# Kernel tuning notes

Hardware: AMD Instinct MI355X
Metric: run time of the kernel (lower is better)

## Reference

```python
import jax, jax.numpy as jnp
import numpy as np
from jax.scipy.special import logsumexp

B, T = 8192, 1024  # batch, timesteps; n_states = 2 (BKT: not-know / know)


def setup_inputs() -> dict:
    key = jax.random.key(0)
    k1, k2, k3 = jax.random.split(key, 3)
    corr = jax.random.randint(k1, (B, T), 0, 2)  # binary observations
    dynamics_logits = jax.random.normal(k2, (B, 3), dtype=jnp.float32)  # (pL, pF, pI0) logits
    obs_logits = jax.random.normal(k3, (B, T, 2), dtype=jnp.float32)  # (pG, pS) logits per step
    return {"corr": corr, "dynamics_logits": dynamics_logits, "obs_logits": obs_logits}


def _get_logits(dynamics_logits, obs_logits):
    # trans_logits[b] = [[0, d1],[d0, 0]]  (target, source)
    z = jnp.zeros_like(dynamics_logits[:, 0])
    trans_logits = jnp.stack([z, dynamics_logits[:, 1], dynamics_logits[:, 0], z], axis=1).reshape(-1, 2, 2)
    # obs_full[b,t] = [[0, o0],[o1, 0]]  (state, output)
    zo = jnp.zeros_like(obs_logits[:, :, 0])
    obs_full = jnp.stack([zo, obs_logits[:, :, 0], obs_logits[:, :, 1], zo], axis=2)
    obs_full = obs_full.reshape(obs_logits.shape[0], -1, 2, 2)
    # init_logits[b] = [0, d2]
    init_logits = jnp.stack([z, dynamics_logits[:, 2]], axis=1)
    return trans_logits, obs_full, init_logits


def _bkt(corr, dynamics_logits, obs_logits):
    trans_logits, obs_full, init_logits = _get_logits(dynamics_logits, obs_logits)
    log_obs = jax.nn.log_softmax(obs_full, axis=3)   # (B,T,2,2)
    log_t = jax.nn.log_softmax(trans_logits, axis=1)  # (B,2,2) softmax over target state
    log_alpha0 = jax.nn.log_softmax(init_logits, axis=1)  # (B,2)
    lo_t = jnp.moveaxis(log_obs, 1, 0)  # (T,B,2,2)
    y_t = corr.T                        # (T,B)

    def fwd_step(log_alpha, inp):
        lo, y = inp  # lo: (B,2,2), y: (B,)
        # predictive p(y_t | y_1:t-1)
        log_py_pred = logsumexp(lo + log_alpha[:, :, None], axis=1)  # (B,2)
        log_py_pred = log_py_pred - logsumexp(log_py_pred, axis=1, keepdims=True)
        # emission of observed symbol per state
        log_py = jnp.take_along_axis(lo, y[:, None, None], axis=2)[:, :, 0]  # (B,2)
        state_post = log_py + log_alpha  # P(h_t, y_1:t)
        new_alpha = logsumexp(log_py[:, None, :] + log_alpha[:, None, :] + log_t, axis=2)
        return new_alpha, (log_py_pred, state_post)

    _, (preds, posts) = jax.lax.scan(fwd_step, log_alpha0, (lo_t, y_t))
    output_logprobs = jnp.moveaxis(preds, 0, 1)     # (B,T,2)
    state_posteriors = jnp.moveaxis(posts, 0, 1)    # (B,T,2)

    def bwd_step(log_beta, inp):
        lo, y = inp
        log_py = jnp.take_along_axis(lo, y[:, None, None], axis=2)[:, :, 0]  # (B,2)
        new_beta = logsumexp(log_py[:, :, None] + log_beta[:, :, None] + log_t, axis=1)
        return new_beta, log_beta

    beta0 = jnp.zeros_like(log_alpha0)
    _, betas = jax.lax.scan(bwd_step, beta0, (lo_t, y_t), reverse=True)
    backward_logprobs = jnp.moveaxis(betas, 0, 1)  # (B,T,2), time-aligned

    smoothed = state_posteriors + backward_logprobs
    smoothed = smoothed - logsumexp(smoothed, axis=2, keepdims=True)
    # stack the three BxTx2 outputs -> (3,B,T,2)
    return jnp.stack([output_logprobs, state_posteriors, smoothed], axis=0)


def reference(corr, dynamics_logits, obs_logits):
    return _bkt(corr, dynamics_logits, obs_logits)
```

## Files before the change

### kernel.cpp

```cpp
#include <hip/hip_runtime.h>


#define BB 8192
#define TT 1024
#define KC 16
#define NC 64
#define GG 4
#define NTHREADS (GG * NC)
#define NEGI (-1.0e30f)

typedef float floatx4 __attribute__((ext_vector_type(4)));

__device__ __forceinline__ float softplusf(float x) {
    return fmaxf(x, 0.0f) + __logf(1.0f + __expf(-fabsf(x)));
}
__device__ __forceinline__ float lse2(float a, float b) {
    float m = fmaxf(a, b);
    return m + __logf(1.0f + __expf(-fabsf(a - b)));
}

__global__ __launch_bounds__(NTHREADS, 3) void bkt_kernel(
        const int* __restrict__ corr,
        const float* __restrict__ dyn,
        const float* __restrict__ obs,
        float* __restrict__ out) {
    __shared__ floatx4 st0[GG][NC][4];
    __shared__ floatx4 st1[GG][NC][4];
    __shared__ floatx4 st2[GG][NC][4];

    const int tid = threadIdx.x;
    const int g = tid >> 6;
    const int c = tid & (NC - 1);
    const int b = blockIdx.x * GG + g;

    const float d0 = dyn[b * 3 + 0];
    const float d1 = dyn[b * 3 + 1];
    const float d2 = dyn[b * 3 + 2];
    const float sd0 = softplusf(d0), sd1 = softplusf(d1);
    const float lt00 = -sd0, lt10 = d0 - sd0, lt01 = d1 - sd1, lt11 = -sd1;

    const long long cb = (long long)b * TT + c * KC;
    const float2* obs2 = (const float2*)obs;
    const long long S4 = (long long)BB * 512;
    floatx4* o0 = (floatx4*)out;
    floatx4* o1 = o0 + S4;
    floatx4* o2 = o1 + S4;

    float ox[16], oy[16], sp0a[16], sp1a[16];
    unsigned ybits = 0;
    float F00, F01, F10, F11;
    {
        const float4* op = (const float4*)(obs2 + cb);
        const int4* yp = (const int4*)(corr + cb);
        #pragma unroll
        for (int j = 0; j < 8; ++j) {
            float4 o4 = op[j];
            ox[2 * j] = o4.x; oy[2 * j] = o4.y;
            ox[2 * j + 1] = o4.z; oy[2 * j + 1] = o4.w;
        }
        #pragma unroll
        for (int j = 0; j < 4; ++j) {
            int4 y4 = yp[j];
            ybits |= (unsigned)(y4.x & 1) << (4 * j + 0);
            ybits |= (unsigned)(y4.y & 1) << (4 * j + 1);
            ybits |= (unsigned)(y4.z & 1) << (4 * j + 2);
            ybits |= (unsigned)(y4.w & 1) << (4 * j + 3);
        }
        #pragma unroll
        for (int q = 0; q < 16; ++q) {
            float sp0 = softplusf(ox[q]), sp1 = softplusf(oy[q]);
            sp0a[q] = sp0; sp1a[q] = sp1;
            int y = (ybits >> q) & 1;
            float py0 = y ? (ox[q] - sp0) : (-sp0);
            float py1 = y ? (-sp1) : (oy[q] - sp1);
            float N00 = py0 + lt00, N01 = py1 + lt01;
            float N10 = py0 + lt10, N11 = py1 + lt11;
            if (q == 0) {
                F00 = N00; F01 = N01; F10 = N10; F11 = N11;
            } else {
                float a_ = lse2(N00 + F00, N01 + F10);
                float b_ = lse2(N00 + F01, N01 + F11);
                float c_ = lse2(N10 + F00, N11 + F10);
                float d_ = lse2(N10 + F01, N11 + F11);
                F00 = a_; F01 = b_; F10 = c_; F11 = d_;
            }
        }
    }

    float G00 = F00, G01 = F01, G10 = F10, G11 = F11;
    float H00 = __shfl_down(F00, 1);
    float H01 = __shfl_down(F10, 1);
    float H10 = __shfl_down(F01, 1);
    float H11 = __shfl_down(F11, 1);
    if (c == NC - 1) { H00 = 0.0f; H01 = NEGI; H10 = NEGI; H11 = 0.0f; }
    #pragma unroll
    for (int dlv = 0; dlv < 6; ++dlv) {
        const int off = 1 << dlv;
        float u00 = __shfl_up(G00, off), u01 = __shfl_up(G01, off);
        float u10 = __shfl_up(G10, off), u11 = __shfl_up(G11, off);
        float g00 = lse2(G00 + u00, G01 + u10);
        float g01 = lse2(G00 + u01, G01 + u11);
        float g10 = lse2(G10 + u00, G11 + u10);
        float g11 = lse2(G10 + u01, G11 + u11);
        bool dg = (c >= off);
        G00 = dg ? g00 : G00; G01 = dg ? g01 : G01;
        G10 = dg ? g10 : G10; G11 = dg ? g11 : G11;
        float v00 = __shfl_down(H00, off), v01 = __shfl_down(H01, off);
        float v10 = __shfl_down(H10, off), v11 = __shfl_down(H11, off);
        float h00 = lse2(H00 + v00, H01 + v10);
        float h01 = lse2(H00 + v01, H01 + v11);
        float h10 = lse2(H10 + v00, H11 + v10);
        float h11 = lse2(H10 + v01, H11 + v11);
        bool dh = (c + off < NC);
        H00 = dh ? h00 : H00; H01 = dh ? h01 : H01;
        H10 = dh ? h10 : H10; H11 = dh ? h11 : H11;
    }
    const float sd2 = softplusf(d2);
    const float ai0 = -sd2, ai1 = d2 - sd2;
    float P00 = __shfl_up(G00, 1), P01 = __shfl_up(G01, 1);
    float P10 = __shfl_up(G10, 1), P11 = __shfl_up(G11, 1);
    float t0 = lse2(P00 + ai0, P01 + ai1);
    float t1 = lse2(P10 + ai0, P11 + ai1);
    float a0 = (c == 0) ? ai0 : t0;
    float a1 = (c == 0) ? ai1 : t1;
    float w0 = lse2(H00, H01);
    float w1 = lse2(H10, H11);
    float be0 = lse2(lt00 + w0, lt10 + w1);
    float be1 = lse2(lt01 + w0, lt11 + w1);

    float bst0[16], bst1[16];
    {
        float bb0 = be0, bb1 = be1;
        #pragma unroll
        for (int q = 15; q >= 0; --q) {
            bst0[q] = bb0; bst1[q] = bb1;
            int y = (ybits >> q) & 1;
            float py0 = y ? (ox[q] - sp0a[q]) : (-sp0a[q]);
            float py1 = y ? (-sp1a[q]) : (oy[q] - sp1a[q]);
            float nb0 = lse2(py0 + bb0 + lt00, py1 + bb1 + lt10);
            float nb1 = lse2(py0 + bb0 + lt01, py1 + bb1 + lt11);
            bb0 = nb0; bb1 = nb1;
        }
    }

    const long long bb4 = (long long)b * 512;
    const int kswz = (c >> 1) & 3;
    #pragma unroll
    for (int h = 0; h < 2; ++h) {
        float e0a, e1a, e0b, e1b, e0c, e1c;
        #pragma unroll
        for (int l = 0; l < 8; ++l) {
            const int q = h * 8 + l;
            float lo00 = -sp0a[q],        lo01 = ox[q] - sp0a[q];
            float lo10 = oy[q] - sp1a[q], lo11 = -sp1a[q];
            float p0 = lse2(lo00 + a0, lo10 + a1);
            float p1 = lse2(lo01 + a0, lo11 + a1);
            float n = lse2(p0, p1);
            float wo0 = p0 - n, wo1 = p1 - n;
            int y = (ybits >> q) & 1;
            float py0 = y ? lo01 : lo00;
            float py1 = y ? lo11 : lo10;
            float s0 = py0 + a0, s1 = py1 + a1;
            float u0 = s0 + bst0[q], u1 = s1 + bst1[q];
            float nn = lse2(u0, u1);
            float w20 = u0 - nn, w21 = u1 - nn;
            a0 = lse2(s0 + lt00, s1 + lt01);
            a1 = lse2(s0 + lt10, s1 + lt11);
            if (l & 1) {
                int kk = (l >> 1) ^ kswz;
                st0[g][c][kk] = (floatx4){e0a, e1a, wo0, wo1};
                st1[g][c][kk] = (floatx4){e0b, e1b, s0, s1};
                st2[g][c][kk] = (floatx4){e0c, e1c, w20, w21};
            } else {
                e0a = wo0; e1a = wo1; e0b = s0; e1b = s1; e0c = w20; e1c = w21;
            }
        }
        #pragma unroll
        for (int i = 0; i < 4; ++i) {
            int flat = i * 64 + c;
            int c2 = flat >> 2, k2 = flat & 3;
            int kk = k2 ^ ((c2 >> 1) & 3);
            long long adr = bb4 + (long long)(c2 * 8 + k2 + 4 * h);
            __builtin_nontemporal_store(st0[g][c2][kk], o0 + adr);
            __builtin_nontemporal_store(st1[g][c2][kk], o1 + adr);
            __builtin_nontemporal_store(st2[g][c2][kk], o2 + adr);
        }
    }
}

extern "C" void kernel_launch(void* const* d_in, const int* in_sizes, int n_in,
                              void* d_out, int out_size, void* d_ws, size_t ws_size,
                              hipStream_t stream) {
    const int*   corr = (const int*)d_in[0];
    const float* dyn  = (const float*)d_in[1];
    const float* obs  = (const float*)d_in[2];
    float* out = (float*)d_out;

    dim3 block(NTHREADS);
    dim3 grid(BB / GG);
    bkt_kernel<<<grid, block, 0, stream>>>(corr, dyn, obs, out);
}
```

Baseline: 294.5 us.

## Recompute softplus and fuse backward pass with smoothed output to cut registers and LDS

Drops the stored softplus arrays and the precomputed per-step backward-beta arrays. Softplus is recomputed where needed, and the backward recursion is folded into a reverse loop that writes the smoothed output, using saved forward state posteriors. Output staging now reuses a single shared buffer, written and drained one output at a time, which cuts LDS to a third. Occupancy launch bounds rise from 3 to 4 blocks per SIMD. The aim is lower register and LDS pressure for higher occupancy, at the cost of extra transcendental work and more staging round trips.

Measured after the change: 320.0 us. 8.6% more time.

```diff
diff --git a/kernel.cpp b/kernel.cpp
--- a/kernel.cpp
+++ b/kernel.cpp
@@ -19,14 +19,12 @@
     return m + __logf(1.0f + __expf(-fabsf(a - b)));
 }
 
-__global__ __launch_bounds__(NTHREADS, 3) void bkt_kernel(
+__global__ __launch_bounds__(NTHREADS, 4) void bkt_kernel(
         const int* __restrict__ corr,
         const float* __restrict__ dyn,
         const float* __restrict__ obs,
         float* __restrict__ out) {
-    __shared__ floatx4 st0[GG][NC][4];
-    __shared__ floatx4 st1[GG][NC][4];
-    __shared__ floatx4 st2[GG][NC][4];
+    __shared__ floatx4 st[GG][NC][4];
 
     const int tid = threadIdx.x;
     const int g = tid >> 6;
@@ -46,7 +44,7 @@
     floatx4* o1 = o0 + S4;
     floatx4* o2 = o1 + S4;
 
-    float ox[16], oy[16], sp0a[16], sp1a[16];
+    float ox[16], oy[16];
     unsigned ybits = 0;
     float F00, F01, F10, F11;
     {
@@ -69,7 +67,6 @@
         #pragma unroll
         for (int q = 0; q < 16; ++q) {
             float sp0 = softplusf(ox[q]), sp1 = softplusf(oy[q]);
-            sp0a[q] = sp0; sp1a[q] = sp1;
             int y = (ybits >> q) & 1;
             float py0 = y ? (ox[q] - sp0) : (-sp0);
             float py1 = y ? (-sp1) : (oy[q] - sp1);
@@ -128,31 +125,19 @@
     float be0 = lse2(lt00 + w0, lt10 + w1);
     float be1 = lse2(lt01 + w0, lt11 + w1);
 
-    float bst0[16], bst1[16];
-    {
-        float bb0 = be0, bb1 = be1;
-        #pragma unroll
-        for (int q = 15; q >= 0; --q) {
-            bst0[q] = bb0; bst1[q] = bb1;
-            int y = (ybits >> q) & 1;
-            float py0 = y ? (ox[q] - sp0a[q]) : (-sp0a[q]);
-            float py1 = y ? (-sp1a[q]) : (oy[q] - sp1a[q]);
-            float nb0 = lse2(py0 + bb0 + lt00, py1 + bb1 + lt10);
-            float nb1 = lse2(py0 + bb0 + lt01, py1 + bb1 + lt11);
-            bb0 = nb0; bb1 = nb1;
-        }
-    }
-
     const long long bb4 = (long long)b * 512;
     const int kswz = (c >> 1) & 3;
+
+    float ps[32];
     #pragma unroll
     for (int h = 0; h < 2; ++h) {
-        float e0a, e1a, e0b, e1b, e0c, e1c;
+        float e0a, e1a;
         #pragma unroll
         for (int l = 0; l < 8; ++l) {
             const int q = h * 8 + l;
-            float lo00 = -sp0a[q],        lo01 = ox[q] - sp0a[q];
-            float lo10 = oy[q] - sp1a[q], lo11 = -sp1a[q];
+            float sp0 = softplusf(ox[q]), sp1 = softplusf(oy[q]);
+            float lo00 = -sp0,        lo01 = ox[q] - sp0;
+            float lo10 = oy[q] - sp1, lo11 = -sp1;
             float p0 = lse2(lo00 + a0, lo10 + a1);
             float p1 = lse2(lo01 + a0, lo11 + a1);
             float n = lse2(p0, p1);
@@ -161,29 +146,61 @@
             float py0 = y ? lo01 : lo00;
             float py1 = y ? lo11 : lo10;
             float s0 = py0 + a0, s1 = py1 + a1;
-            float u0 = s0 + bst0[q], u1 = s1 + bst1[q];
-            float nn = lse2(u0, u1);
-            float w20 = u0 - nn, w21 = u1 - nn;
+            ps[2 * q] = s0; ps[2 * q + 1] = s1;
             a0 = lse2(s0 + lt00, s1 + lt01);
             a1 = lse2(s0 + lt10, s1 + lt11);
             if (l & 1) {
-                int kk = (l >> 1) ^ kswz;
-                st0[g][c][kk] = (floatx4){e0a, e1a, wo0, wo1};
-                st1[g][c][kk] = (floatx4){e0b, e1b, s0, s1};
-                st2[g][c][kk] = (floatx4){e0c, e1c, w20, w21};
-            } else {
-                e0a = wo0; e1a = wo1; e0b = s0; e1b = s1; e0c = w20; e1c = w21;
-            }
+                st[g][c][(l >> 1) ^ kswz] = (floatx4){e0a, e1a, wo0, wo1};
+            } else { e0a = wo0; e1a = wo1; }
         }
         #pragma unroll
         for (int i = 0; i < 4; ++i) {
             int flat = i * 64 + c;
             int c2 = flat >> 2, k2 = flat & 3;
-            int kk = k2 ^ ((c2 >> 1) & 3);
-            long long adr = bb4 + (long long)(c2 * 8 + k2 + 4 * h);
-            __builtin_nontemporal_store(st0[g][c2][kk], o0 + adr);
-            __builtin_nontemporal_store(st1[g][c2][kk], o1 + adr);
-            __builtin_nontemporal_store(st2[g][c2][kk], o2 + adr);
+            floatx4 v = st[g][c2][k2 ^ ((c2 >> 1) & 3)];
+            __builtin_nontemporal_store(
+                v, o0 + bb4 + (long long)(c2 * 8 + k2 + 4 * h));
+        }
+        #pragma unroll
+        for (int k = 0; k < 4; ++k)
+            st[g][c][k ^ kswz] = (floatx4){ps[16 * h + 4 * k], ps[16 * h + 4 * k + 1],
+                                           ps[16 * h + 4 * k + 2], ps[16 * h + 4 * k + 3]};
+        #pragma unroll
+        for (int i = 0; i < 4; ++i) {
+            int flat = i * 64 + c;
+            int c2 = flat >> 2, k2 = flat & 3;
+            floatx4 v = st[g][c2][k2 ^ ((c2 >> 1) & 3)];
+            __builtin_nontemporal_store(
+                v, o1 + bb4 + (long long)(c2 * 8 + k2 + 4 * h));
+        }
+    }
+
+    #pragma unroll
+    for (int h = 1; h >= 0; --h) {
+        float o0s, o1s;
+        #pragma unroll
+        for (int l = 7; l >= 0; --l) {
+            const int q = h * 8 + l;
+            float u0 = ps[2 * q] + be0, u1 = ps[2 * q + 1] + be1;
+            float nn = lse2(u0, u1);
+            float w20 = u0 - nn, w21 = u1 - nn;
+            float sp0 = softplusf(ox[q]), sp1 = softplusf(oy[q]);
+            int y = (ybits >> q) & 1;
+            float py0 = y ? (ox[q] - sp0) : (-sp0);
+            float py1 = y ? (-sp1) : (oy[q] - sp1);
+            float nb0 = lse2(py0 + be0 + lt00, py1 + be1 + lt10);
+            float nb1 = lse2(py0 + be0 + lt01, py1 + be1 + lt11);
+            be0 = nb0; be1 = nb1;
+            if (l & 1) { o0s = w20; o1s = w21; }
+            else       st[g][c][(l >> 1) ^ kswz] = (floatx4){w20, w21, o0s, o1s};
+        }
+        #pragma unroll
+        for (int i = 0; i < 4; ++i) {
+            int flat = i * 64 + c;
+            int c2 = flat >> 2, k2 = flat & 3;
+            floatx4 v = st[g][c2][k2 ^ ((c2 >> 1) & 3)];
+            __builtin_nontemporal_store(
+                v, o2 + bb4 + (long long)(c2 * 8 + k2 + 4 * h));
         }
     }
 }
```
